# Kernel tuning notes

Measured on AMD Instinct MI355X. Metric: run time of the kernel, lower is better.

The kernel has to match this reference:

```python
import jax, jax.numpy as jnp
import numpy as np

BN, C, P = 1024, 32, 7          # patches, feat channels, patch size
G, MAX_DISP, DS = 8, 160, 1     # groups, max disparity, downsample rate
D = MAX_DISP // DS              # disparity bins = hypergraph nodes N
K, TH = 3, 16                   # kNN k, spatial threshold
W = P + MAX_DISP                # right strip width
NEG = -1e9


def setup_inputs() -> dict:
    key = jax.random.key(0)
    ks = jax.random.split(key, 7)
    left_feat = jax.random.normal(ks[0], (BN, C, P, P), jnp.float32)
    right_feat = jax.random.normal(ks[1], (BN, C, P, W), jnp.float32)
    start_left = jax.random.randint(ks[2], (BN,), 0, MAX_DISP + 1)
    f1_w = jax.random.normal(ks[3], (G, G), jnp.float32) / np.sqrt(G)
    f1_b = jax.random.normal(ks[4], (G,), jnp.float32) * 0.01
    conv_w = jax.random.normal(ks[5], (1, G, 3), jnp.float32) / np.sqrt(3 * G)
    conv_b = jax.random.normal(ks[6], (1,), jnp.float32) * 0.01
    return dict(left_feat=left_feat, right_feat=right_feat, start_left=start_left,
                f1_w=f1_w, f1_b=f1_b, conv_w=conv_w, conv_b=conv_b)


def _square_distance(src, dst):
    d = -2.0 * jnp.einsum('bnc,bmc->bnm', src, dst)
    return d + jnp.sum(src ** 2, -1)[:, :, None] + jnp.sum(dst ** 2, -1)[:, None, :]


def _mean_agg(X, path):
    # X' = path @ X, then mean-normalize rows; 1/0 -> 0 as in torch (isinf -> 0)
    out = jnp.einsum('brc,bcf->brf', path, X)
    s = jnp.sum(path, axis=2, keepdims=True)
    return jnp.where(s > 0, out / jnp.where(s > 0, s, 1.0), 0.0)


def _hypconv(x, H, f1_w, f1_b):
    # Linear -> LeakyReLU -> Dropout(eval: identity) -> v2e -> e2v
    h = jax.nn.leaky_relu(x @ f1_w.T + f1_b, 0.01)
    E = _mean_agg(h, jnp.swapaxes(H, 1, 2))
    return _mean_agg(E, H)


def _forward(left_feat, right_feat, f1_w, f1_b, conv_w, conv_b, start_left):
    bn = left_feat.shape[0]
    d_vals = jnp.arange(D) * DS
    # group-wise correlation cost volume: right window at column start_left - d
    cols = start_left[:, None, None] - d_vals[None, :, None] + jnp.arange(P)[None, None, :]  # [bn,D,P]
    valid = jnp.all((cols >= 0) & (cols < W), axis=2).astype(left_feat.dtype)                # [bn,D]
    cols_c = jnp.clip(cols, 0, W - 1).reshape(bn, 1, 1, D * P)
    r = jnp.take_along_axis(right_feat, cols_c, axis=3).reshape(bn, C, P, D, P)
    lg = left_feat.reshape(bn, G, C // G, P, P)
    rg = r.reshape(bn, G, C // G, P, D, P)
    vol = jnp.einsum('bgcyx,bgcydx->bgd', lg, rg) / (C // G * P * P)
    vol = vol * valid[:, None, :]                          # [bn,G,D]
    mask = jnp.sum(vol, axis=1, keepdims=True) == 0        # [bn,1,D]

    feature = jnp.swapaxes(vol, 1, 2)                      # [bn,D,G] nodes x feats
    _, idx = jax.lax.top_k(-_square_distance(feature, feature), K)  # k smallest dists, [bn,D,K]
    pos = jnp.arange(D)[None, :, None]
    near = jnp.abs(idx - pos) < TH
    row_pos = jnp.where(near, idx, D)                      # far neighbors -> dummy row D
    row_neg = jnp.where(near, D, idx)
    b_i = jnp.arange(bn)[:, None, None]
    c_i = jnp.arange(D)[None, :, None]
    hg_pos = jnp.zeros((bn, D + 1, D), feature.dtype).at[b_i, row_pos, c_i].set(1.0)[:, :D, :]
    hg_neg = jnp.zeros((bn, D + 1, D), feature.dtype).at[b_i, row_neg, c_i].set(1.0)[:, :D, :]

    # HGNNPN: note the original uses hgconv1 for BOTH branches (hgconv2 is dead)
    x1 = _hypconv(feature, hg_pos, f1_w, f1_b)
    x2 = _hypconv(feature, hg_neg, f1_w, f1_b)
    feat = feature + 0.1 * x1 - 0.1 * x2

    cv = jnp.swapaxes(feat, 1, 2)                          # [bn,G,D]
    agg = jax.lax.conv_general_dilated(cv, conv_w, (1,), [(1, 1)],
                                       dimension_numbers=('NCH', 'OIH', 'NCH'))
    agg = agg + conv_b[None, :, None]
    agg = jnp.where(mask, NEG, agg)
    prob = jax.nn.softmax(agg, axis=2).reshape(bn, -1)
    return jnp.sum(prob * d_vals.astype(prob.dtype), axis=1) * DS


def reference(left_feat, right_feat, start_left, f1_w, f1_b, conv_w, conv_b):
    return _forward(left_feat, right_feat, f1_w, f1_b, conv_w, conv_b, start_left)
```

## Files before the change

### kernel.cpp

```cpp
#include <hip/hip_runtime.h>
#include <math.h>

#define TBN 1024
#define TC  32
#define TP  7
#define TG  8
#define TD  160
#define TW  167
#define TK  3
#define TTH 16
#define CPG 4
#define NEGV -1e9f

typedef float f4 __attribute__((ext_vector_type(4)));

__global__ __launch_bounds__(256, 4)
void patchmix_kernel(const float* __restrict__ left,
                     const float* __restrict__ right,
                     const int*   __restrict__ start_left,
                     const float* __restrict__ f1w,
                     const float* __restrict__ f1b,
                     const float* __restrict__ convw,
                     const float* __restrict__ convb,
                     float* __restrict__ out)
{
    __shared__ __align__(16) float s_pool[2880];
    __shared__ __align__(16) float s_feat[TD][TG];
    __shared__ float s_h[TD * 9];
    __shared__ float s_norm[TD];
    __shared__ float s_agg[TD];
    __shared__ float s_f1w[TG * TG];
    __shared__ float s_f1b[TG];
    __shared__ float s_cw[TG * 3];
    __shared__ float s_cb;
    __shared__ int   s_idx[TD][TK];
    __shared__ int   s_near[TD][TK];
    __shared__ int   s_degP[TD];
    __shared__ int   s_degN[TD];

    float* const s_lp   = s_pool;
    float* const s_accP = s_pool;
    float* const s_accN = s_pool + 1440;

    const int bn = blockIdx.x;
    const int t  = threadIdx.x;
    const int start = start_left[bn];

    {
        const float* lsrc = left + bn * (TC * TP * TP);
        for (int i = t; i < TC * TP * TP; i += 256) {
            const int cy = i / 7;
            const int x  = i - cy * 7;
            s_lp[cy * 8 + x] = lsrc[i];
        }
        if (t < 64)        s_f1w[t]      = f1w[t];
        else if (t < 72)   s_f1b[t - 64] = f1b[t - 64];
        else if (t < 96)   s_cw[t - 72]  = convw[t - 72];
        else if (t == 96)  s_cb          = convb[0];
    }
    __syncthreads();

    {
        const int g  = t >> 5;
        const int d0 = (t & 31) * 5;
        float a0 = 0.f, a1 = 0.f, a2 = 0.f, a3 = 0.f, a4 = 0.f;
        if (d0 <= start) {
            const int col0 = start - d0 - 4;
            const float* rp = right + ((bn * TC + g * CPG) * TP) * TW + col0;
            const float* lq = s_lp + g * (CPG * TP) * 8;
            const int o0 = (col0 >=  0) ? 0 : 4;
            const int o1 = (col0 >= -1) ? 1 : 4;
            const int o2 = (col0 >= -2) ? 2 : 4;
            const int o3 = (col0 >= -3) ? 3 : 4;
            float w0,w1,w2,w3,w4,w5,w6,w7,w8,w9,w10;
            float x0,x1,x2,x3,x4,x5,x6,x7,x8,x9,x10;
#define LOADW(b0,b1,b2,b3,b4,b5,b6,b7,b8,b9,b10,p) \
            b0=(p)[o0]; b1=(p)[o1]; b2=(p)[o2]; b3=(p)[o3]; b4=(p)[4]; \
            b5=(p)[5]; b6=(p)[6]; b7=(p)[7]; b8=(p)[8]; b9=(p)[9]; b10=(p)[10];
#define FMA5(la,lb,r0,r1,r2,r3,r4,r5,r6,r7,r8,r9,r10) \
            a0=fmaf(la.x,r4,a0);  a0=fmaf(la.y,r5,a0);  a0=fmaf(la.z,r6,a0); \
            a0=fmaf(la.w,r7,a0);  a0=fmaf(lb.x,r8,a0);  a0=fmaf(lb.y,r9,a0); \
            a0=fmaf(lb.z,r10,a0); \
            a1=fmaf(la.x,r3,a1);  a1=fmaf(la.y,r4,a1);  a1=fmaf(la.z,r5,a1); \
            a1=fmaf(la.w,r6,a1);  a1=fmaf(lb.x,r7,a1);  a1=fmaf(lb.y,r8,a1); \
            a1=fmaf(lb.z,r9,a1); \
            a2=fmaf(la.x,r2,a2);  a2=fmaf(la.y,r3,a2);  a2=fmaf(la.z,r4,a2); \
            a2=fmaf(la.w,r5,a2);  a2=fmaf(lb.x,r6,a2);  a2=fmaf(lb.y,r7,a2); \
            a2=fmaf(lb.z,r8,a2); \
            a3=fmaf(la.x,r1,a3);  a3=fmaf(la.y,r2,a3);  a3=fmaf(la.z,r3,a3); \
            a3=fmaf(la.w,r4,a3);  a3=fmaf(lb.x,r5,a3);  a3=fmaf(lb.y,r6,a3); \
            a3=fmaf(lb.z,r7,a3); \
            a4=fmaf(la.x,r0,a4);  a4=fmaf(la.y,r1,a4);  a4=fmaf(la.z,r2,a4); \
            a4=fmaf(la.w,r3,a4);  a4=fmaf(lb.x,r4,a4);  a4=fmaf(lb.y,r5,a4); \
            a4=fmaf(lb.z,r6,a4);

            LOADW(w0,w1,w2,w3,w4,w5,w6,w7,w8,w9,w10, rp)
            for (int h = 0; h < 14; ++h) {
                const f4 la0 = *(const f4*)(lq);
                const f4 lb0 = *(const f4*)(lq + 4);
                const f4 la1 = *(const f4*)(lq + 8);
                const f4 lb1 = *(const f4*)(lq + 12);
                LOADW(x0,x1,x2,x3,x4,x5,x6,x7,x8,x9,x10, rp + TW)
                FMA5(la0, lb0, w0,w1,w2,w3,w4,w5,w6,w7,w8,w9,w10)
                rp += 2 * TW;
                if (h < 13) {
                    LOADW(w0,w1,w2,w3,w4,w5,w6,w7,w8,w9,w10, rp)
                }
                FMA5(la1, lb1, x0,x1,x2,x3,x4,x5,x6,x7,x8,x9,x10)
                lq += 16;
            }
#undef LOADW
#undef FMA5
        }
        s_feat[d0 + 0][g] = (d0 + 0 <= start) ? a0 / 196.0f : 0.f;
        s_feat[d0 + 1][g] = (d0 + 1 <= start) ? a1 / 196.0f : 0.f;
        s_feat[d0 + 2][g] = (d0 + 2 <= start) ? a2 / 196.0f : 0.f;
        s_feat[d0 + 3][g] = (d0 + 3 <= start) ? a3 / 196.0f : 0.f;
        s_feat[d0 + 4][g] = (d0 + 4 <= start) ? a4 / 196.0f : 0.f;
    }
    __syncthreads();

    if (t < TD) {
        float s = 0.f;
#pragma unroll
        for (int g = 0; g < TG; ++g) { float v = s_feat[t][g]; s = fmaf(v, v, s); }
        s_norm[t] = s;
    }
    __syncthreads();

    if (t < TD) {
        const f4 fa = ((const f4*)s_feat[t])[0];
        const f4 fb = ((const f4*)s_feat[t])[1];
        const float ni = s_norm[t];
        float v0 = 3e38f, v1 = 3e38f, v2 = 3e38f;
        int   i0 = -1,    i1 = -1,    i2 = -1;
        for (int j = 0; j < TD; ++j) {
            const f4 ga = ((const f4*)s_feat[j])[0];
            const f4 gb = ((const f4*)s_feat[j])[1];
            float dot = fa.x * ga.x + fa.y * ga.y + fa.z * ga.z + fa.w * ga.w
                      + fb.x * gb.x + fb.y * gb.y + fb.z * gb.z + fb.w * gb.w;
            float dist = ni + s_norm[j] - 2.f * dot;
            if (dist < v2) {
                v2 = dist; i2 = j;
                if (v2 < v1) {
                    float tv = v1; v1 = v2; v2 = tv; int ti = i1; i1 = i2; i2 = ti;
                    if (v1 < v0) {
                        tv = v0; v0 = v1; v1 = tv; ti = i0; i0 = i1; i1 = ti;
                    }
                }
            }
        }
        s_idx[t][0] = i0; s_idx[t][1] = i1; s_idx[t][2] = i2;
        int dk0 = i0 - t, dk1 = i1 - t, dk2 = i2 - t;
        s_near[t][0] = (dk0 < TTH && dk0 > -TTH);
        s_near[t][1] = (dk1 < TTH && dk1 > -TTH);
        s_near[t][2] = (dk2 < TTH && dk2 > -TTH);
    } else {
        for (int i = t - TD; i < 2880; i += 96) s_pool[i] = 0.f;
        for (int i = t - TD; i < TD;   i += 96) { s_degP[i] = 0; s_degN[i] = 0; }
    }
    __syncthreads();

    for (int task = t; task < TD * TG; task += 256) {
        const int d = task >> 3, go = task & 7;
        float s = s_f1b[go];
#pragma unroll
        for (int gi = 0; gi < TG; ++gi) s = fmaf(s_feat[d][gi], s_f1w[go * TG + gi], s);
        s_h[d * 9 + go] = (s >= 0.f) ? s : 0.01f * s;
    }
    __syncthreads();

    if (t < TD) {
        const int jj[3] = { s_idx[t][0], s_idx[t][1], s_idx[t][2] };
        const int nr[3] = { s_near[t][0], s_near[t][1], s_near[t][2] };
        float ep[TG] = {0, 0, 0, 0, 0, 0, 0, 0};
        float en[TG] = {0, 0, 0, 0, 0, 0, 0, 0};
        int cp = 0, cn = 0;
#pragma unroll
        for (int k = 0; k < TK; ++k) {
            const float* hp = &s_h[jj[k] * 9];
            if (nr[k]) { cp++;
#pragma unroll
                for (int g = 0; g < TG; ++g) ep[g] += hp[g];
            } else { cn++;
#pragma unroll
                for (int g = 0; g < TG; ++g) en[g] += hp[g];
            }
        }
        if (cp) {
#pragma unroll
            for (int g = 0; g < TG; ++g) ep[g] /= (float)cp;
        }
        if (cn) {
#pragma unroll
            for (int g = 0; g < TG; ++g) en[g] /= (float)cn;
        }
#pragma unroll
        for (int k = 0; k < TK; ++k) {
            if (nr[k]) {
                atomicAdd(&s_degP[jj[k]], 1);
#pragma unroll
                for (int g = 0; g < TG; ++g) atomicAdd(&s_accP[jj[k] * 9 + g], ep[g]);
            } else {
                atomicAdd(&s_degN[jj[k]], 1);
#pragma unroll
                for (int g = 0; g < TG; ++g) atomicAdd(&s_accN[jj[k] * 9 + g], en[g]);
            }
        }
    }
    __syncthreads();

    if (t < TD) {
        const int dp = s_degP[t], dn = s_degN[t];
#pragma unroll
        for (int g = 0; g < TG; ++g) {
            float x1 = dp ? s_accP[t * 9 + g] / (float)dp : 0.f;
            float x2 = dn ? s_accN[t * 9 + g] / (float)dn : 0.f;
            s_accP[t * 9 + g] = s_feat[t][g] + 0.1f * x1 - 0.1f * x2;
        }
    }
    __syncthreads();

    if (t < TD) {
        float msum = 0.f;
#pragma unroll
        for (int g = 0; g < TG; ++g) msum += s_feat[t][g];
        float a = s_cb;
#pragma unroll
        for (int kw = 0; kw < 3; ++kw) {
            const int dd = t + kw - 1;
            if (dd >= 0 && dd < TD) {
#pragma unroll
                for (int g = 0; g < TG; ++g)
                    a = fmaf(s_accP[dd * 9 + g], s_cw[g * 3 + kw], a);
            }
        }
        s_agg[t] = (msum == 0.f) ? NEGV : a;
    }
    __syncthreads();

    if (t < 64) {
        float m = -3e38f;
        for (int d = t; d < TD; d += 64) m = fmaxf(m, s_agg[d]);
#pragma unroll
        for (int off = 32; off; off >>= 1) m = fmaxf(m, __shfl_xor(m, off, 64));
        float se = 0.f, sd = 0.f;
        for (int d = t; d < TD; d += 64) {
            float e = expf(s_agg[d] - m);
            se += e;
            sd = fmaf(e, (float)d, sd);
        }
#pragma unroll
        for (int off = 32; off; off >>= 1) {
            se += __shfl_xor(se, off, 64);
            sd += __shfl_xor(sd, off, 64);
        }
        if (t == 0) out[bn] = sd / se;
    }
}

extern "C" void kernel_launch(void* const* d_in, const int* in_sizes, int n_in,
                              void* d_out, int out_size, void* d_ws, size_t ws_size,
                              hipStream_t stream) {
    const float* left   = (const float*)d_in[0];
    const float* right  = (const float*)d_in[1];
    const int*   start  = (const int*)d_in[2];
    const float* f1w    = (const float*)d_in[3];
    const float* f1b    = (const float*)d_in[4];
    const float* convw  = (const float*)d_in[5];
    const float* convb  = (const float*)d_in[6];
    float* out = (float*)d_out;
    patchmix_kernel<<<TBN, 256, 0, stream>>>(left, right, start, f1w, f1b,
                                             convw, convb, out);
}
```

Before: 289.2 us.

## Split cost-volume stage into separate kernel with more, smaller blocks

Splits the fused kernel in two. The first kernel computes the group-wise correlation cost volume over 2048 blocks of 128 threads, each handling half the groups, and writes the features to workspace memory. The second kernel reads them back and runs the kNN, hypergraph convolution and softmax regression. The aim is to raise parallelism and occupancy for the memory-heavy correlation phase, which no longer shares the large hypergraph LDS footprint. In exchange it adds a global round trip for the features and a second launch.

```diff
diff --git a/kernel.cpp b/kernel.cpp
--- a/kernel.cpp
+++ b/kernel.cpp
@@ -14,19 +14,101 @@
 
 typedef float f4 __attribute__((ext_vector_type(4)));
 
+__global__ __launch_bounds__(128, 8)
+void costvol_kernel(const float* __restrict__ left,
+                    const float* __restrict__ right,
+                    const int*   __restrict__ start_left,
+                    float* __restrict__ feat)
+{
+    __shared__ float s_lp[4 * 28 * 8];
+
+    const int blk   = blockIdx.x;
+    const int bn    = blk >> 1;
+    const int gbase = (blk & 1) * 4;
+    const int t     = threadIdx.x;
+    const int start = start_left[bn];
+
+    {
+        const float* lsrc = left + bn * (TC * TP * TP) + gbase * CPG * TP * TP;
+        for (int i = t; i < 784; i += 128) {
+            const int cy = i / 7;
+            const int x  = i - cy * 7;
+            s_lp[cy * 8 + x] = lsrc[i];
+        }
+    }
+    __syncthreads();
+
+    const int gl = t >> 5;
+    const int d0 = (t & 31) * 5;
+    float a0 = 0.f, a1 = 0.f, a2 = 0.f, a3 = 0.f, a4 = 0.f;
+    if (d0 <= start) {
+        const int col0 = start - d0 - 4;
+        const float* rp = right + ((bn * TC + (gbase + gl) * CPG) * TP) * TW + col0;
+        const float* lq = s_lp + gl * (CPG * TP) * 8;
+        const int o0 = (col0 >=  0) ? 0 : 4;
+        const int o1 = (col0 >= -1) ? 1 : 4;
+        const int o2 = (col0 >= -2) ? 2 : 4;
+        const int o3 = (col0 >= -3) ? 3 : 4;
+        float w0,w1,w2,w3,w4,w5,w6,w7,w8,w9,w10;
+        float x0,x1,x2,x3,x4,x5,x6,x7,x8,x9,x10;
+#define LOADW(b0,b1,b2,b3,b4,b5,b6,b7,b8,b9,b10,p) \
+        b0=(p)[o0]; b1=(p)[o1]; b2=(p)[o2]; b3=(p)[o3]; b4=(p)[4]; \
+        b5=(p)[5]; b6=(p)[6]; b7=(p)[7]; b8=(p)[8]; b9=(p)[9]; b10=(p)[10];
+#define FMA5(la,lb,r0,r1,r2,r3,r4,r5,r6,r7,r8,r9,r10) \
+        a0=fmaf(la.x,r4,a0);  a0=fmaf(la.y,r5,a0);  a0=fmaf(la.z,r6,a0); \
+        a0=fmaf(la.w,r7,a0);  a0=fmaf(lb.x,r8,a0);  a0=fmaf(lb.y,r9,a0); \
+        a0=fmaf(lb.z,r10,a0); \
+        a1=fmaf(la.x,r3,a1);  a1=fmaf(la.y,r4,a1);  a1=fmaf(la.z,r5,a1); \
+        a1=fmaf(la.w,r6,a1);  a1=fmaf(lb.x,r7,a1);  a1=fmaf(lb.y,r8,a1); \
+        a1=fmaf(lb.z,r9,a1); \
+        a2=fmaf(la.x,r2,a2);  a2=fmaf(la.y,r3,a2);  a2=fmaf(la.z,r4,a2); \
+        a2=fmaf(la.w,r5,a2);  a2=fmaf(lb.x,r6,a2);  a2=fmaf(lb.y,r7,a2); \
+        a2=fmaf(lb.z,r8,a2); \
+        a3=fmaf(la.x,r1,a3);  a3=fmaf(la.y,r2,a3);  a3=fmaf(la.z,r3,a3); \
+        a3=fmaf(la.w,r4,a3);  a3=fmaf(lb.x,r5,a3);  a3=fmaf(lb.y,r6,a3); \
+        a3=fmaf(lb.z,r7,a3); \
+        a4=fmaf(la.x,r0,a4);  a4=fmaf(la.y,r1,a4);  a4=fmaf(la.z,r2,a4); \
+        a4=fmaf(la.w,r3,a4);  a4=fmaf(lb.x,r4,a4);  a4=fmaf(lb.y,r5,a4); \
+        a4=fmaf(lb.z,r6,a4);
+
+        LOADW(w0,w1,w2,w3,w4,w5,w6,w7,w8,w9,w10, rp)
+        for (int h = 0; h < 14; ++h) {
+            const f4 la0 = *(const f4*)(lq);
+            const f4 lb0 = *(const f4*)(lq + 4);
+            const f4 la1 = *(const f4*)(lq + 8);
+            const f4 lb1 = *(const f4*)(lq + 12);
+            LOADW(x0,x1,x2,x3,x4,x5,x6,x7,x8,x9,x10, rp + TW)
+            FMA5(la0, lb0, w0,w1,w2,w3,w4,w5,w6,w7,w8,w9,w10)
+            rp += 2 * TW;
+            if (h < 13) {
+                LOADW(w0,w1,w2,w3,w4,w5,w6,w7,w8,w9,w10, rp)
+            }
+            FMA5(la1, lb1, x0,x1,x2,x3,x4,x5,x6,x7,x8,x9,x10)
+            lq += 16;
+        }
+#undef LOADW
+#undef FMA5
+    }
+    float* fp = feat + bn * (TD * TG) + gbase + gl;
+    fp[(d0 + 0) * TG] = (d0 + 0 <= start) ? a0 / 196.0f : 0.f;
+    fp[(d0 + 1) * TG] = (d0 + 1 <= start) ? a1 / 196.0f : 0.f;
+    fp[(d0 + 2) * TG] = (d0 + 2 <= start) ? a2 / 196.0f : 0.f;
+    fp[(d0 + 3) * TG] = (d0 + 3 <= start) ? a3 / 196.0f : 0.f;
+    fp[(d0 + 4) * TG] = (d0 + 4 <= start) ? a4 / 196.0f : 0.f;
+}
+
 __global__ __launch_bounds__(256, 4)
-void patchmix_kernel(const float* __restrict__ left,
-                     const float* __restrict__ right,
-                     const int*   __restrict__ start_left,
-                     const float* __restrict__ f1w,
-                     const float* __restrict__ f1b,
-                     const float* __restrict__ convw,
-                     const float* __restrict__ convb,
-                     float* __restrict__ out)
+void hyper_kernel(const float* __restrict__ feat,
+                  const float* __restrict__ f1w,
+                  const float* __restrict__ f1b,
+                  const float* __restrict__ convw,
+                  const float* __restrict__ convb,
+                  float* __restrict__ out)
 {
-    __shared__ __align__(16) float s_pool[2880];
     __shared__ __align__(16) float s_feat[TD][TG];
     __shared__ float s_h[TD * 9];
+    __shared__ float s_accP[TD * 9];
+    __shared__ float s_accN[TD * 9];
     __shared__ float s_norm[TD];
     __shared__ float s_agg[TD];
     __shared__ float s_f1w[TG * TG];
@@ -38,85 +120,18 @@
     __shared__ int   s_degP[TD];
     __shared__ int   s_degN[TD];
 
-    float* const s_lp   = s_pool;
-    float* const s_accP = s_pool;
-    float* const s_accN = s_pool + 1440;
-
     const int bn = blockIdx.x;
     const int t  = threadIdx.x;
-    const int start = start_left[bn];
 
     {
-        const float* lsrc = left + bn * (TC * TP * TP);
-        for (int i = t; i < TC * TP * TP; i += 256) {
-            const int cy = i / 7;
-            const int x  = i - cy * 7;
-            s_lp[cy * 8 + x] = lsrc[i];
-        }
+        const float* fsrc = feat + bn * (TD * TG);
+        for (int i = t; i < TD * TG; i += 256) ((float*)s_feat)[i] = fsrc[i];
+        for (int i = t; i < TD * 9; i += 256) { s_accP[i] = 0.f; s_accN[i] = 0.f; }
         if (t < 64)        s_f1w[t]      = f1w[t];
         else if (t < 72)   s_f1b[t - 64] = f1b[t - 64];
         else if (t < 96)   s_cw[t - 72]  = convw[t - 72];
         else if (t == 96)  s_cb          = convb[0];
-    }
-    __syncthreads();
-
-    {
-        const int g  = t >> 5;
-        const int d0 = (t & 31) * 5;
-        float a0 = 0.f, a1 = 0.f, a2 = 0.f, a3 = 0.f, a4 = 0.f;
-        if (d0 <= start) {
-            const int col0 = start - d0 - 4;
-            const float* rp = right + ((bn * TC + g * CPG) * TP) * TW + col0;
-            const float* lq = s_lp + g * (CPG * TP) * 8;
-            const int o0 = (col0 >=  0) ? 0 : 4;
-            const int o1 = (col0 >= -1) ? 1 : 4;
-            const int o2 = (col0 >= -2) ? 2 : 4;
-            const int o3 = (col0 >= -3) ? 3 : 4;
-            float w0,w1,w2,w3,w4,w5,w6,w7,w8,w9,w10;
-            float x0,x1,x2,x3,x4,x5,x6,x7,x8,x9,x10;
-#define LOADW(b0,b1,b2,b3,b4,b5,b6,b7,b8,b9,b10,p) \
-            b0=(p)[o0]; b1=(p)[o1]; b2=(p)[o2]; b3=(p)[o3]; b4=(p)[4]; \
-            b5=(p)[5]; b6=(p)[6]; b7=(p)[7]; b8=(p)[8]; b9=(p)[9]; b10=(p)[10];
-#define FMA5(la,lb,r0,r1,r2,r3,r4,r5,r6,r7,r8,r9,r10) \
-            a0=fmaf(la.x,r4,a0);  a0=fmaf(la.y,r5,a0);  a0=fmaf(la.z,r6,a0); \
-            a0=fmaf(la.w,r7,a0);  a0=fmaf(lb.x,r8,a0);  a0=fmaf(lb.y,r9,a0); \
-            a0=fmaf(lb.z,r10,a0); \
-            a1=fmaf(la.x,r3,a1);  a1=fmaf(la.y,r4,a1);  a1=fmaf(la.z,r5,a1); \
-            a1=fmaf(la.w,r6,a1);  a1=fmaf(lb.x,r7,a1);  a1=fmaf(lb.y,r8,a1); \
-            a1=fmaf(lb.z,r9,a1); \
-            a2=fmaf(la.x,r2,a2);  a2=fmaf(la.y,r3,a2);  a2=fmaf(la.z,r4,a2); \
-            a2=fmaf(la.w,r5,a2);  a2=fmaf(lb.x,r6,a2);  a2=fmaf(lb.y,r7,a2); \
-            a2=fmaf(lb.z,r8,a2); \
-            a3=fmaf(la.x,r1,a3);  a3=fmaf(la.y,r2,a3);  a3=fmaf(la.z,r3,a3); \
-            a3=fmaf(la.w,r4,a3);  a3=fmaf(lb.x,r5,a3);  a3=fmaf(lb.y,r6,a3); \
-            a3=fmaf(lb.z,r7,a3); \
-            a4=fmaf(la.x,r0,a4);  a4=fmaf(la.y,r1,a4);  a4=fmaf(la.z,r2,a4); \
-            a4=fmaf(la.w,r3,a4);  a4=fmaf(lb.x,r4,a4);  a4=fmaf(lb.y,r5,a4); \
-            a4=fmaf(lb.z,r6,a4);
-
-            LOADW(w0,w1,w2,w3,w4,w5,w6,w7,w8,w9,w10, rp)
-            for (int h = 0; h < 14; ++h) {
-                const f4 la0 = *(const f4*)(lq);
-                const f4 lb0 = *(const f4*)(lq + 4);
-                const f4 la1 = *(const f4*)(lq + 8);
-                const f4 lb1 = *(const f4*)(lq + 12);
-                LOADW(x0,x1,x2,x3,x4,x5,x6,x7,x8,x9,x10, rp + TW)
-                FMA5(la0, lb0, w0,w1,w2,w3,w4,w5,w6,w7,w8,w9,w10)
-                rp += 2 * TW;
-                if (h < 13) {
-                    LOADW(w0,w1,w2,w3,w4,w5,w6,w7,w8,w9,w10, rp)
-                }
-                FMA5(la1, lb1, x0,x1,x2,x3,x4,x5,x6,x7,x8,x9,x10)
-                lq += 16;
-            }
-#undef LOADW
-#undef FMA5
-        }
-        s_feat[d0 + 0][g] = (d0 + 0 <= start) ? a0 / 196.0f : 0.f;
-        s_feat[d0 + 1][g] = (d0 + 1 <= start) ? a1 / 196.0f : 0.f;
-        s_feat[d0 + 2][g] = (d0 + 2 <= start) ? a2 / 196.0f : 0.f;
-        s_feat[d0 + 3][g] = (d0 + 3 <= start) ? a3 / 196.0f : 0.f;
-        s_feat[d0 + 4][g] = (d0 + 4 <= start) ? a4 / 196.0f : 0.f;
+        else if (t >= 128 && t < 128 + TD) { s_degP[t - 128] = 0; s_degN[t - 128] = 0; }
     }
     __syncthreads();
 
@@ -155,9 +170,6 @@
         s_near[t][0] = (dk0 < TTH && dk0 > -TTH);
         s_near[t][1] = (dk1 < TTH && dk1 > -TTH);
         s_near[t][2] = (dk2 < TTH && dk2 > -TTH);
-    } else {
-        for (int i = t - TD; i < 2880; i += 96) s_pool[i] = 0.f;
-        for (int i = t - TD; i < TD;   i += 96) { s_degP[i] = 0; s_degN[i] = 0; }
     }
     __syncthreads();
 
@@ -269,7 +281,9 @@
     const float* f1b    = (const float*)d_in[4];
     const float* convw  = (const float*)d_in[5];
     const float* convb  = (const float*)d_in[6];
-    float* out = (float*)d_out;
-    patchmix_kernel<<<TBN, 256, 0, stream>>>(left, right, start, f1w, f1b,
-                                             convw, convb, out);
+    float* out  = (float*)d_out;
+    float* feat = (float*)d_ws;
+
+    costvol_kernel<<<TBN * 2, 128, 0, stream>>>(left, right, start, feat);
+    hyper_kernel<<<TBN, 256, 0, stream>>>(feat, f1w, f1b, convw, convb, out);
 }
```

Result: slower. 312.4 us (+8.0%).
